# Kernel optimization log

Hardware: AMD Instinct MI355X
Metric: run time of the kernel (lower is better)

The kernel has to match this reference:

```python
import jax, jax.numpy as jnp
import numpy as np

EPS = 1e-6
LN_EPS = 1e-6


def _bd(x, W):
    # Block-diagonal dense: x (B, F) viewed as (B, H, D); W (H, D, D)
    B = x.shape[0]
    H, D, _ = W.shape
    return jnp.einsum('bhd,hde->bhe', x.reshape(B, H, D), W).reshape(B, H * D)


def setup_inputs() -> dict:
    key = jax.random.key(0)
    B, F, H, D, K = 4096, 1024, 4, 256, 4
    ks = jax.random.split(key, 24)
    inp = {}
    inp['inputs'] = jax.random.normal(ks[0], (B, F), jnp.float32)
    inp['c'] = jax.random.normal(ks[1], (B, F), jnp.float32)
    inp['n'] = jax.random.uniform(ks[2], (B, F), jnp.float32)  # nonzero -> general stabilizer branch
    inp['m'] = jax.random.normal(ks[3], (B, F), jnp.float32)
    inp['h'] = jax.random.normal(ks[4], (B, F), jnp.float32)
    inp['conv_state'] = jax.random.normal(ks[5], (B, K, F), jnp.float32)
    inp['conv_kernel'] = jax.random.normal(ks[6], (K, F), jnp.float32) * 0.1
    inp['conv_bias'] = jax.random.normal(ks[7], (F,), jnp.float32) * 0.1
    for idx, name in enumerate(['Wi', 'Wf', 'Wz', 'Wo', 'Ri', 'Rf', 'Rz', 'Ro']):
        inp[name] = jax.random.normal(ks[8 + idx], (H, D, D), jnp.float32) * 0.02
    for idx, name in enumerate(['bi', 'bf', 'bz', 'bo']):
        inp[name] = jax.random.normal(ks[16 + idx], (F,), jnp.float32) * 0.1
    inp['ln_scale'] = jnp.ones((H, D), jnp.float32)
    return inp


def reference(inputs, c, n, m, h, conv_state, conv_kernel, conv_bias,
              Wi, Wf, Wz, Wo, Ri, Rf, Rz, Ro, bi, bf, bz, bo, ln_scale):
    B = inputs.shape[0]
    H, D = ln_scale.shape

    # Causal depthwise conv, single step: shift state, append new input
    new_conv_state = jnp.concatenate([conv_state[:, 1:, :], inputs[:, None, :]], axis=1)  # (B,K,F)
    conv_x = jnp.einsum('bkf,kf->bf', new_conv_state, conv_kernel) + conv_bias
    conv_act = jax.nn.silu(conv_x)

    # Gate pre-activations: input (block-diag) + recurrent (block-diag) + bias
    i = _bd(conv_act, Wi) + _bd(h, Ri) + bi
    f = _bd(conv_act, Wf) + _bd(h, Rf) + bf
    z = _bd(inputs, Wz) + _bd(h, Rz) + bz
    o = _bd(inputs, Wo) + _bd(h, Ro) + bo

    o_gate = jax.nn.sigmoid(o)
    log_f = -jax.nn.softplus(-f)  # forget_activation == 'sigmoid'

    # Stabilizer
    m_new = jnp.where(jnp.all(n == 0.0), i, jnp.maximum(log_f + m, i))
    i_p = jnp.minimum(jnp.exp(i - m_new), 1.0)
    f_p = jnp.minimum(jnp.exp(log_f + m - m_new), 1.0)

    c_new = f_p * c + i_p * jnp.tanh(z)
    n_new = f_p * n + i_p
    h_new = o_gate * (c_new / jnp.maximum(n_new, EPS))

    # Multi-head LayerNorm over head_dim (scale only, no bias)
    y = h_new.reshape(B, H, D)
    mu = jnp.mean(y, axis=-1, keepdims=True)
    var = jnp.var(y, axis=-1, keepdims=True)
    out = ((y - mu) * jax.lax.rsqrt(var + LN_EPS) * ln_scale).reshape(B, H * D)

    return (out, c_new, n_new, m_new, h_new, new_conv_state)
```

## Files before the change

### kernel.cpp

```cpp
#include <hip/hip_runtime.h>

#define B_N 4096
#define F_N 1024
#define H_N 4
#define D_N 256
#define BF_ELEMS (B_N * F_N)

typedef unsigned short u16;
typedef __bf16 bf16x8 __attribute__((ext_vector_type(8)));
typedef float f32x4 __attribute__((ext_vector_type(4)));
typedef u16 u16x4 __attribute__((ext_vector_type(4)));

__device__ __forceinline__ u16 f2bf(float v) {
    union { float f; unsigned u; } x; x.f = v;
    unsigned r = x.u + 0x7fffu + ((x.u >> 16) & 1u);
    return (u16)(r >> 16);
}

__device__ __forceinline__ float bf2f(u16 v) {
    union { unsigned u; float f; } x; x.u = ((unsigned)v) << 16;
    return x.f;
}

__global__ __launch_bounds__(256) void kprep(
    const float* __restrict__ inputs, const float* __restrict__ cs,
    const float* __restrict__ ck, const float* __restrict__ cb,
    const float* __restrict__ h, const float* __restrict__ n,
    const float* W0, const float* W1, const float* W2, const float* W3,
    const float* W4, const float* W5, const float* W6, const float* W7,
    float* __restrict__ ncs_out, u16* __restrict__ convact,
    u16* __restrict__ hbf, u16* __restrict__ inbf,
    u16* __restrict__ wt, int* __restrict__ flag) {
    __shared__ float tile[32][33];
    int bid = blockIdx.x;
    int t = threadIdx.x;
    if (bid < 4096) {
        int idx = bid * 256 + t;
        int flat = idx << 2;
        int b = flat >> 10;
        int f = flat & 1023;
        const f32x4 x  = *(const f32x4*)(inputs + flat);
        const f32x4 c1 = *(const f32x4*)(cs + b * 4096 + 1024 + f);
        const f32x4 c2 = *(const f32x4*)(cs + b * 4096 + 2048 + f);
        const f32x4 c3 = *(const f32x4*)(cs + b * 4096 + 3072 + f);
        const f32x4 k0 = *(const f32x4*)(ck + f);
        const f32x4 k1 = *(const f32x4*)(ck + 1024 + f);
        const f32x4 k2 = *(const f32x4*)(ck + 2048 + f);
        const f32x4 k3 = *(const f32x4*)(ck + 3072 + f);
        const f32x4 bias = *(const f32x4*)(cb + f);
        const f32x4 h4 = *(const f32x4*)(h + flat);
        const f32x4 nv = *(const f32x4*)(n + flat);

        bool any = (nv[0] != 0.f) || (nv[1] != 0.f) || (nv[2] != 0.f) || (nv[3] != 0.f);
        unsigned long long msk = __ballot(any);
        if (msk && (t & 63) == 0) *flag = 1;

        u16x4 ca, hb, ib;
        #pragma unroll
        for (int q = 0; q < 4; ++q) {
            float v = c1[q] * k0[q] + c2[q] * k1[q] + c3[q] * k2[q] + x[q] * k3[q] + bias[q];
            float a = v / (1.f + expf(-v));
            ca[q] = f2bf(a);
            hb[q] = f2bf(h4[q]);
            ib[q] = f2bf(x[q]);
        }
        *(u16x4*)(convact + flat) = ca;
        *(u16x4*)(hbf + flat) = hb;
        *(u16x4*)(inbf + flat) = ib;

        float* ob = ncs_out + b * 4096 + f;
        *(f32x4*)(ob)        = c1;
        *(f32x4*)(ob + 1024) = c2;
        *(f32x4*)(ob + 2048) = c3;
        *(f32x4*)(ob + 3072) = x;
    } else {
        int wb = bid - 4096;
        int gx = wb & 63;
        int hd = (wb >> 6) & 3;
        int mat = wb >> 8;
        const float* tab[8] = {W0, W1, W2, W3, W4, W5, W6, W7};
        const float* src = tab[mat] + hd * 65536;
        u16* dst = wt + (mat * 4 + hd) * 65536;
        int tx = t & 31, ty = t >> 5;
        int bx = (gx & 7) * 32;
        int by = (gx >> 3) * 32;
        #pragma unroll
        for (int r = 0; r < 4; ++r)
            tile[ty + r * 8][tx] = src[(by + ty + r * 8) * 256 + bx + tx];
        __syncthreads();
        #pragma unroll
        for (int r = 0; r < 4; ++r)
            dst[(bx + ty + r * 8) * 256 + by + tx] = f2bf(tile[tx][ty + r * 8]);
    }
}

__global__ __launch_bounds__(512, 4) void kgemm(
    const u16* __restrict__ convact, const u16* __restrict__ inbf,
    const u16* __restrict__ hbf, const u16* __restrict__ wt,
    const float* __restrict__ bgi, const float* __restrict__ bgf,
    const float* __restrict__ bgz, const float* __restrict__ bgo,
    u16* __restrict__ gates16) {
    __shared__ u16 ldsA[128 * 64];
    __shared__ u16 ldsB[256 * 64];

    int t = threadIdx.x;
    int mtile = blockIdx.x;
    int pairidx = blockIdx.y;
    int gsel = pairidx >> 2;
    int hd = pairidx & 3;
    int row0 = mtile * 128;

    const u16* a0 = (gsel >= 2 ? inbf : convact) + row0 * 1024 + hd * 256;
    const u16* a1 = hbf + row0 * 1024 + hd * 256;
    const u16* b0 = wt + (gsel * 4 + hd) * 65536;
    const u16* b1 = wt + ((gsel + 4) * 4 + hd) * 65536;
    const float* bias = (gsel == 0 ? bgi : gsel == 1 ? bgf : gsel == 2 ? bgz : bgo) + hd * 256;

    f32x4 acc[4][4];
    #pragma unroll
    for (int i = 0; i < 4; ++i)
        #pragma unroll
        for (int j = 0; j < 4; ++j)
            acc[i][j] = (f32x4){0.f, 0.f, 0.f, 0.f};

    int lane = t & 63;
    int lr = lane & 15, lk = lane >> 4;
    int w = t >> 6;
    int wm = w >> 2, wn = w & 3;
    int wbase = t & ~63;

    int arow = t >> 3, aseg = t & 7;

    for (int ks = 0; ks < 8; ++ks) {
        int kb = ks * 64;
        const u16* ap = (kb < 256) ? (a0 + kb) : (a1 + (kb - 256));
        const u16* bp = (kb < 256) ? (b0 + kb) : (b1 + (kb - 256));
        __syncthreads();
        #pragma unroll
        for (int s = 0; s < 2; ++s) {
            int row = arow + s * 64;
            __builtin_amdgcn_global_load_lds(
                (const __attribute__((address_space(1))) void*)(ap + row * 1024 + aseg * 8),
                (__attribute__((address_space(3))) void*)(&ldsA[(wbase + s * 512) * 8]),
                16, 0, 0);
        }
        #pragma unroll
        for (int s = 0; s < 4; ++s) {
            int row = arow + s * 64;
            __builtin_amdgcn_global_load_lds(
                (const __attribute__((address_space(1))) void*)(bp + row * 256 + aseg * 8),
                (__attribute__((address_space(3))) void*)(&ldsB[(wbase + s * 512) * 8]),
                16, 0, 0);
        }
        __syncthreads();

        #pragma unroll
        for (int kk = 0; kk < 2; ++kk) {
            bf16x8 a[4], bfr[4];
            #pragma unroll
            for (int mi = 0; mi < 4; ++mi)
                a[mi] = *(const bf16x8*)&ldsA[(wm * 64 + mi * 16 + lr) * 64 + kk * 32 + lk * 8];
            #pragma unroll
            for (int ni = 0; ni < 4; ++ni)
                bfr[ni] = *(const bf16x8*)&ldsB[(wn * 64 + ni * 16 + lr) * 64 + kk * 32 + lk * 8];
            #pragma unroll
            for (int mi = 0; mi < 4; ++mi)
                #pragma unroll
                for (int ni = 0; ni < 4; ++ni)
                    acc[mi][ni] = __builtin_amdgcn_mfma_f32_16x16x32_bf16(a[mi], bfr[ni], acc[mi][ni], 0, 0, 0);
        }
    }

    float bv[4];
    #pragma unroll
    for (int ni = 0; ni < 4; ++ni)
        bv[ni] = bias[wn * 64 + ni * 16 + lr];

    u16* gout = gates16 + (size_t)gsel * BF_ELEMS;
    #pragma unroll
    for (int mi = 0; mi < 4; ++mi)
        #pragma unroll
        for (int ni = 0; ni < 4; ++ni)
            #pragma unroll
            for (int r = 0; r < 4; ++r) {
                int row = row0 + wm * 64 + mi * 16 + lk * 4 + r;
                int col = hd * 256 + wn * 64 + ni * 16 + lr;
                gout[row * 1024 + col] = f2bf(acc[mi][ni][r] + bv[ni]);
            }
}

__global__ __launch_bounds__(256) void kpoint(
    const u16* __restrict__ gates16,
    const float* __restrict__ c, const float* __restrict__ n, const float* __restrict__ m,
    const float* __restrict__ ln_scale, const int* __restrict__ flagp,
    float* __restrict__ out) {
    int b = blockIdx.x;
    int t = threadIdx.x;
    int l = t & 63;
    int j = (t >> 6) * 256 + l * 4;
    int idx = b * 1024 + j;
    int flag = *flagp;

    u16x4 iv = *(const u16x4*)(gates16 + idx);
    u16x4 fv = *(const u16x4*)(gates16 + (size_t)BF_ELEMS + idx);
    u16x4 zv = *(const u16x4*)(gates16 + 2 * (size_t)BF_ELEMS + idx);
    u16x4 ov = *(const u16x4*)(gates16 + 3 * (size_t)BF_ELEMS + idx);
    f32x4 cv = *(const f32x4*)(c + idx);
    f32x4 nv = *(const f32x4*)(n + idx);
    f32x4 mv = *(const f32x4*)(m + idx);
    f32x4 sc = *(const f32x4*)(ln_scale + j);

    f32x4 cn, nn, mn, hn;
    float s = 0.f, ss = 0.f;
    #pragma unroll
    for (int q = 0; q < 4; ++q) {
        float I = bf2f(iv[q]);
        float Fg = bf2f(fv[q]);
        float Z = bf2f(zv[q]);
        float O = bf2f(ov[q]);
        float og = 1.f / (1.f + expf(-O));
        float lf = (Fg >= 0.f) ? -log1pf(expf(-Fg)) : (Fg - log1pf(expf(Fg)));
        float mnew = flag ? fmaxf(lf + mv[q], I) : I;
        float ip = fminf(expf(I - mnew), 1.f);
        float fp = fminf(expf(lf + mv[q] - mnew), 1.f);
        float cnew = fp * cv[q] + ip * tanhf(Z);
        float nnew = fp * nv[q] + ip;
        float hnew = og * (cnew / fmaxf(nnew, 1e-6f));
        cn[q] = cnew; nn[q] = nnew; mn[q] = mnew; hn[q] = hnew;
        s += hnew; ss += hnew * hnew;
    }
    #pragma unroll
    for (int off = 32; off >= 1; off >>= 1) {
        s  += __shfl_xor(s, off);
        ss += __shfl_xor(ss, off);
    }
    float mu = s * (1.f / 256.f);
    float var = ss * (1.f / 256.f) - mu * mu;
    float rs = rsqrtf(var + 1e-6f);

    f32x4 o4;
    #pragma unroll
    for (int q = 0; q < 4; ++q)
        o4[q] = (hn[q] - mu) * rs * sc[q];

    *(f32x4*)(out + idx) = o4;
    *(f32x4*)(out + (size_t)BF_ELEMS + idx) = cn;
    *(f32x4*)(out + 2 * (size_t)BF_ELEMS + idx) = nn;
    *(f32x4*)(out + 3 * (size_t)BF_ELEMS + idx) = mn;
    *(f32x4*)(out + 4 * (size_t)BF_ELEMS + idx) = hn;
}

extern "C" void kernel_launch(void* const* d_in, const int* in_sizes, int n_in,
                              void* d_out, int out_size, void* d_ws, size_t ws_size,
                              hipStream_t stream) {
    const float* inputs = (const float*)d_in[0];
    const float* c = (const float*)d_in[1];
    const float* n = (const float*)d_in[2];
    const float* m = (const float*)d_in[3];
    const float* h = (const float*)d_in[4];
    const float* conv_state = (const float*)d_in[5];
    const float* conv_kernel = (const float*)d_in[6];
    const float* conv_bias = (const float*)d_in[7];
    const float* W[8];
    for (int i = 0; i < 8; ++i) W[i] = (const float*)d_in[8 + i];
    const float* bgi = (const float*)d_in[16];
    const float* bgf = (const float*)d_in[17];
    const float* bgz = (const float*)d_in[18];
    const float* bgo = (const float*)d_in[19];
    const float* ln_scale = (const float*)d_in[20];
    float* out = (float*)d_out;

    char* ws = (char*)d_ws;
    int* flag = (int*)ws;
    u16* convact = (u16*)(ws + 256);
    u16* hbf = convact + BF_ELEMS;
    u16* inbf = hbf + BF_ELEMS;
    u16* wt = inbf + BF_ELEMS;
    u16* gates16 = wt + (size_t)8 * 4 * 65536;

    hipMemsetAsync(flag, 0, 4, stream);
    kprep<<<6144, 256, 0, stream>>>(inputs, conv_state, conv_kernel, conv_bias, h, n,
                                    W[0], W[1], W[2], W[3], W[4], W[5], W[6], W[7],
                                    out + 5 * (size_t)BF_ELEMS, convact, hbf, inbf, wt, flag);
    kgemm<<<dim3(32, 16), 512, 0, stream>>>(convact, inbf, hbf, wt,
                                            bgi, bgf, bgz, bgo, gates16);
    kpoint<<<4096, 256, 0, stream>>>(gates16, c, n, m, ln_scale, flag, out);
}
```

Baseline: 114.4 us.

## Double-buffer GEMM LDS tiles, enlarge M tile to 256, add XOR swizzle

The gate GEMM kernel now prefetches the next K tile into a second LDS buffer while computing on the current one, removing one barrier per iteration. The M tile doubles to 256 rows per block, so each wave handles 8x4 MFMA tiles and half as many blocks launch. An XOR swizzle on the LDS column segments is meant to avoid bank conflicts on fragment reads. In exchange it uses 128KB of LDS, more accumulator registers and lower occupancy (launch bounds cut to 2), and only 256 blocks run across the CUs.

```diff
diff --git a/kernel.cpp b/kernel.cpp
--- a/kernel.cpp
+++ b/kernel.cpp
@@ -94,21 +94,21 @@
     }
 }
 
-__global__ __launch_bounds__(512, 4) void kgemm(
+__global__ __launch_bounds__(512, 2) void kgemm(
     const u16* __restrict__ convact, const u16* __restrict__ inbf,
     const u16* __restrict__ hbf, const u16* __restrict__ wt,
     const float* __restrict__ bgi, const float* __restrict__ bgf,
     const float* __restrict__ bgz, const float* __restrict__ bgo,
     u16* __restrict__ gates16) {
-    __shared__ u16 ldsA[128 * 64];
-    __shared__ u16 ldsB[256 * 64];
+    __shared__ u16 ldsA[2][256 * 64];
+    __shared__ u16 ldsB[2][256 * 64];
 
     int t = threadIdx.x;
     int mtile = blockIdx.x;
     int pairidx = blockIdx.y;
     int gsel = pairidx >> 2;
     int hd = pairidx & 3;
-    int row0 = mtile * 128;
+    int row0 = mtile * 256;
 
     const u16* a0 = (gsel >= 2 ? inbf : convact) + row0 * 1024 + hd * 256;
     const u16* a1 = hbf + row0 * 1024 + hd * 256;
@@ -116,9 +116,9 @@
     const u16* b1 = wt + ((gsel + 4) * 4 + hd) * 65536;
     const float* bias = (gsel == 0 ? bgi : gsel == 1 ? bgf : gsel == 2 ? bgz : bgo) + hd * 256;
 
-    f32x4 acc[4][4];
-    #pragma unroll
-    for (int i = 0; i < 4; ++i)
+    f32x4 acc[8][4];
+    #pragma unroll
+    for (int i = 0; i < 8; ++i)
         #pragma unroll
         for (int j = 0; j < 4; ++j)
             acc[i][j] = (f32x4){0.f, 0.f, 0.f, 0.f};
@@ -128,47 +128,58 @@
     int w = t >> 6;
     int wm = w >> 2, wn = w & 3;
     int wbase = t & ~63;
-
-    int arow = t >> 3, aseg = t & 7;
-
-    for (int ks = 0; ks < 8; ++ks) {
-        int kb = ks * 64;
-        const u16* ap = (kb < 256) ? (a0 + kb) : (a1 + (kb - 256));
-        const u16* bp = (kb < 256) ? (b0 + kb) : (b1 + (kb - 256));
-        __syncthreads();
-        #pragma unroll
-        for (int s = 0; s < 2; ++s) {
-            int row = arow + s * 64;
-            __builtin_amdgcn_global_load_lds(
-                (const __attribute__((address_space(1))) void*)(ap + row * 1024 + aseg * 8),
-                (__attribute__((address_space(3))) void*)(&ldsA[(wbase + s * 512) * 8]),
-                16, 0, 0);
-        }
-        #pragma unroll
-        for (int s = 0; s < 4; ++s) {
-            int row = arow + s * 64;
-            __builtin_amdgcn_global_load_lds(
-                (const __attribute__((address_space(1))) void*)(bp + row * 256 + aseg * 8),
-                (__attribute__((address_space(3))) void*)(&ldsB[(wbase + s * 512) * 8]),
-                16, 0, 0);
+    int srow = t >> 3;
+    int gsw = (t & 7) ^ ((t >> 3) & 7);
+
+    #define STAGE_TILE(buf, kt) do {                                              \
+        int kb = (kt) * 64;                                                       \
+        const u16* ap = (kb < 256) ? (a0 + kb) : (a1 + (kb - 256));               \
+        const u16* bp = (kb < 256) ? (b0 + kb) : (b1 + (kb - 256));               \
+        _Pragma("unroll")                                                         \
+        for (int s = 0; s < 4; ++s) {                                             \
+            int row = srow + s * 64;                                              \
+            __builtin_amdgcn_global_load_lds(                                     \
+                (const __attribute__((address_space(1))) void*)(ap + row * 1024 + gsw * 8), \
+                (__attribute__((address_space(3))) void*)(&ldsA[buf][(s * 512 + wbase) * 8]), \
+                16, 0, 0);                                                        \
+        }                                                                         \
+        _Pragma("unroll")                                                         \
+        for (int s = 0; s < 4; ++s) {                                             \
+            int row = srow + s * 64;                                              \
+            __builtin_amdgcn_global_load_lds(                                     \
+                (const __attribute__((address_space(1))) void*)(bp + row * 256 + gsw * 8), \
+                (__attribute__((address_space(3))) void*)(&ldsB[buf][(s * 512 + wbase) * 8]), \
+                16, 0, 0);                                                        \
+        }                                                                         \
+    } while (0)
+
+    STAGE_TILE(0, 0);
+    __syncthreads();
+
+    for (int kt = 0; kt < 8; ++kt) {
+        int buf = kt & 1;
+        if (kt < 7) STAGE_TILE(buf ^ 1, kt + 1);
+
+        #pragma unroll
+        for (int kk = 0; kk < 2; ++kk) {
+            bf16x8 a[8], bb[4];
+            #pragma unroll
+            for (int mi = 0; mi < 8; ++mi) {
+                int row = wm * 128 + mi * 16 + lr;
+                a[mi] = *(const bf16x8*)&ldsA[buf][row * 64 + (((kk * 4 + lk) ^ (lr & 7)) * 8)];
+            }
+            #pragma unroll
+            for (int ni = 0; ni < 4; ++ni) {
+                int row = wn * 64 + ni * 16 + lr;
+                bb[ni] = *(const bf16x8*)&ldsB[buf][row * 64 + (((kk * 4 + lk) ^ (lr & 7)) * 8)];
+            }
+            #pragma unroll
+            for (int mi = 0; mi < 8; ++mi)
+                #pragma unroll
+                for (int ni = 0; ni < 4; ++ni)
+                    acc[mi][ni] = __builtin_amdgcn_mfma_f32_16x16x32_bf16(a[mi], bb[ni], acc[mi][ni], 0, 0, 0);
         }
         __syncthreads();
-
-        #pragma unroll
-        for (int kk = 0; kk < 2; ++kk) {
-            bf16x8 a[4], bfr[4];
-            #pragma unroll
-            for (int mi = 0; mi < 4; ++mi)
-                a[mi] = *(const bf16x8*)&ldsA[(wm * 64 + mi * 16 + lr) * 64 + kk * 32 + lk * 8];
-            #pragma unroll
-            for (int ni = 0; ni < 4; ++ni)
-                bfr[ni] = *(const bf16x8*)&ldsB[(wn * 64 + ni * 16 + lr) * 64 + kk * 32 + lk * 8];
-            #pragma unroll
-            for (int mi = 0; mi < 4; ++mi)
-                #pragma unroll
-                for (int ni = 0; ni < 4; ++ni)
-                    acc[mi][ni] = __builtin_amdgcn_mfma_f32_16x16x32_bf16(a[mi], bfr[ni], acc[mi][ni], 0, 0, 0);
-        }
     }
 
     float bv[4];
@@ -178,15 +189,16 @@
 
     u16* gout = gates16 + (size_t)gsel * BF_ELEMS;
     #pragma unroll
-    for (int mi = 0; mi < 4; ++mi)
+    for (int mi = 0; mi < 8; ++mi)
         #pragma unroll
         for (int ni = 0; ni < 4; ++ni)
             #pragma unroll
             for (int r = 0; r < 4; ++r) {
-                int row = row0 + wm * 64 + mi * 16 + lk * 4 + r;
+                int row = row0 + wm * 128 + mi * 16 + lk * 4 + r;
                 int col = hd * 256 + wn * 64 + ni * 16 + lr;
                 gout[row * 1024 + col] = f2bf(acc[mi][ni][r] + bv[ni]);
             }
+    #undef STAGE_TILE
 }
 
 __global__ __launch_bounds__(256) void kpoint(
@@ -282,7 +294,7 @@
     kprep<<<6144, 256, 0, stream>>>(inputs, conv_state, conv_kernel, conv_bias, h, n,
                                     W[0], W[1], W[2], W[3], W[4], W[5], W[6], W[7],
                                     out + 5 * (size_t)BF_ELEMS, convact, hbf, inbf, wt, flag);
-    kgemm<<<dim3(32, 16), 512, 0, stream>>>(convact, inbf, hbf, wt,
+    kgemm<<<dim3(16, 16), 512, 0, stream>>>(convact, inbf, hbf, wt,
                                             bgi, bgf, bgz, bgo, gates16);
     kpoint<<<4096, 256, 0, stream>>>(gates16, c, n, m, ln_scale, flag, out);
 }
```

New measurement: 112.4 us. No clear change (-1.7%).

## Fuse gate GEMMs with pointwise cell update and LayerNorm per head tile

Applied to the files above, without the earlier changes.

Merges the gate GEMM and pointwise kernels into one kernel. Each block computes all four gates for a 32-row by one-head tile, stages the bf16 gate values in LDS, then runs the stabilized cell update and per-head LayerNorm directly. This removes the global round trip of the bf16 gates buffer and one kernel launch. Weights are rearranged into k-chunked panels and read straight from global/L2 into registers rather than through LDS. Activations are loaded once into swizzled LDS. The cost is that every block re-reads the full weight panels from cache, and the grid is smaller with 1024-thread blocks.

```diff
diff --git a/kernel.cpp b/kernel.cpp
--- a/kernel.cpp
+++ b/kernel.cpp
@@ -10,6 +10,7 @@
 typedef __bf16 bf16x8 __attribute__((ext_vector_type(8)));
 typedef float f32x4 __attribute__((ext_vector_type(4)));
 typedef u16 u16x4 __attribute__((ext_vector_type(4)));
+typedef u16 u16x8 __attribute__((ext_vector_type(8)));
 
 __device__ __forceinline__ u16 f2bf(float v) {
     union { float f; unsigned u; } x; x.f = v;
@@ -90,164 +91,180 @@
         __syncthreads();
         #pragma unroll
         for (int r = 0; r < 4; ++r)
-            dst[(bx + ty + r * 8) * 256 + by + tx] = f2bf(tile[tx][ty + r * 8]);
-    }
-}
-
-__global__ __launch_bounds__(512, 4) void kgemm(
+            dst[(by >> 5) * 8192 + (bx + ty + r * 8) * 32 + tx] = f2bf(tile[tx][ty + r * 8]);
+    }
+}
+
+__global__ __launch_bounds__(1024, 4) void kfused(
     const u16* __restrict__ convact, const u16* __restrict__ inbf,
-    const u16* __restrict__ hbf, const u16* __restrict__ wt,
+    const u16* __restrict__ hbf, const u16* __restrict__ wt2,
     const float* __restrict__ bgi, const float* __restrict__ bgf,
     const float* __restrict__ bgz, const float* __restrict__ bgo,
-    u16* __restrict__ gates16) {
-    __shared__ u16 ldsA[128 * 64];
-    __shared__ u16 ldsB[256 * 64];
+    const float* __restrict__ c, const float* __restrict__ n,
+    const float* __restrict__ m, const float* __restrict__ ln_scale,
+    const int* __restrict__ flagp, float* __restrict__ out) {
+    __shared__ __align__(16) u16 smem[32768];
 
     int t = threadIdx.x;
     int mtile = blockIdx.x;
-    int pairidx = blockIdx.y;
-    int gsel = pairidx >> 2;
-    int hd = pairidx & 3;
-    int row0 = mtile * 128;
-
-    const u16* a0 = (gsel >= 2 ? inbf : convact) + row0 * 1024 + hd * 256;
-    const u16* a1 = hbf + row0 * 1024 + hd * 256;
-    const u16* b0 = wt + (gsel * 4 + hd) * 65536;
-    const u16* b1 = wt + ((gsel + 4) * 4 + hd) * 65536;
-    const float* bias = (gsel == 0 ? bgi : gsel == 1 ? bgf : gsel == 2 ? bgz : bgo) + hd * 256;
-
-    f32x4 acc[4][4];
+    int hd = blockIdx.y;
+    int row0 = mtile * 32;
+
+    {
+        int r = t >> 5, gd = t & 31;
+        int gl = gd ^ (r & 7);
+        size_t soff = (size_t)(row0 + r) * 1024 + hd * 256 + gl * 8;
+        __builtin_amdgcn_global_load_lds(
+            (const __attribute__((address_space(1))) void*)(convact + soff),
+            (__attribute__((address_space(3))) void*)(&smem[t * 8]), 16, 0, 0);
+        __builtin_amdgcn_global_load_lds(
+            (const __attribute__((address_space(1))) void*)(inbf + soff),
+            (__attribute__((address_space(3))) void*)(&smem[8192 + t * 8]), 16, 0, 0);
+        __builtin_amdgcn_global_load_lds(
+            (const __attribute__((address_space(1))) void*)(hbf + soff),
+            (__attribute__((address_space(3))) void*)(&smem[16384 + t * 8]), 16, 0, 0);
+    }
+    __syncthreads();
+
+    int lane = t & 63, lr = lane & 15, lk = lane >> 4;
+    int w = t >> 6;
+    int g = w >> 2;
+    int q = w & 3;
+
+    f32x4 acc[2][4];
     #pragma unroll
-    for (int i = 0; i < 4; ++i)
+    for (int i = 0; i < 2; ++i)
         #pragma unroll
         for (int j = 0; j < 4; ++j)
             acc[i][j] = (f32x4){0.f, 0.f, 0.f, 0.f};
 
-    int lane = t & 63;
-    int lr = lane & 15, lk = lane >> 4;
-    int w = t >> 6;
-    int wm = w >> 2, wn = w & 3;
-    int wbase = t & ~63;
-
-    int arow = t >> 3, aseg = t & 7;
-
+    const u16* bW = wt2 + (size_t)(g * 4 + hd) * 65536;
+    const u16* bR = wt2 + (size_t)((g + 4) * 4 + hd) * 65536;
+    int bcol = (q * 64 + lr) * 32 + lk * 8;
+    int aselW = (g < 2) ? 0 : 8192;
+    int grs = (lr & 7);
+
+    #pragma unroll 4
     for (int ks = 0; ks < 8; ++ks) {
-        int kb = ks * 64;
-        const u16* ap = (kb < 256) ? (a0 + kb) : (a1 + (kb - 256));
-        const u16* bp = (kb < 256) ? (b0 + kb) : (b1 + (kb - 256));
-        __syncthreads();
-        #pragma unroll
-        for (int s = 0; s < 2; ++s) {
-            int row = arow + s * 64;
-            __builtin_amdgcn_global_load_lds(
-                (const __attribute__((address_space(1))) void*)(ap + row * 1024 + aseg * 8),
-                (__attribute__((address_space(3))) void*)(&ldsA[(wbase + s * 512) * 8]),
-                16, 0, 0);
-        }
-        #pragma unroll
-        for (int s = 0; s < 4; ++s) {
-            int row = arow + s * 64;
-            __builtin_amdgcn_global_load_lds(
-                (const __attribute__((address_space(1))) void*)(bp + row * 256 + aseg * 8),
-                (__attribute__((address_space(3))) void*)(&ldsB[(wbase + s * 512) * 8]),
-                16, 0, 0);
-        }
-        __syncthreads();
-
-        #pragma unroll
-        for (int kk = 0; kk < 2; ++kk) {
-            bf16x8 a[4], bfr[4];
+        bf16x8 b0 = *(const bf16x8*)(bW + ks * 8192 + bcol);
+        bf16x8 b1 = *(const bf16x8*)(bW + ks * 8192 + bcol + 512);
+        bf16x8 b2 = *(const bf16x8*)(bW + ks * 8192 + bcol + 1024);
+        bf16x8 b3 = *(const bf16x8*)(bW + ks * 8192 + bcol + 1536);
+        int gr = (ks * 4 + lk) ^ grs;
+        bf16x8 a0 = *(const bf16x8*)&smem[aselW + lr * 256 + gr * 8];
+        bf16x8 a1 = *(const bf16x8*)&smem[aselW + (16 + lr) * 256 + gr * 8];
+        acc[0][0] = __builtin_amdgcn_mfma_f32_16x16x32_bf16(a0, b0, acc[0][0], 0, 0, 0);
+        acc[0][1] = __builtin_amdgcn_mfma_f32_16x16x32_bf16(a0, b1, acc[0][1], 0, 0, 0);
+        acc[0][2] = __builtin_amdgcn_mfma_f32_16x16x32_bf16(a0, b2, acc[0][2], 0, 0, 0);
+        acc[0][3] = __builtin_amdgcn_mfma_f32_16x16x32_bf16(a0, b3, acc[0][3], 0, 0, 0);
+        acc[1][0] = __builtin_amdgcn_mfma_f32_16x16x32_bf16(a1, b0, acc[1][0], 0, 0, 0);
+        acc[1][1] = __builtin_amdgcn_mfma_f32_16x16x32_bf16(a1, b1, acc[1][1], 0, 0, 0);
+        acc[1][2] = __builtin_amdgcn_mfma_f32_16x16x32_bf16(a1, b2, acc[1][2], 0, 0, 0);
+        acc[1][3] = __builtin_amdgcn_mfma_f32_16x16x32_bf16(a1, b3, acc[1][3], 0, 0, 0);
+    }
+    #pragma unroll 4
+    for (int ks = 0; ks < 8; ++ks) {
+        bf16x8 b0 = *(const bf16x8*)(bR + ks * 8192 + bcol);
+        bf16x8 b1 = *(const bf16x8*)(bR + ks * 8192 + bcol + 512);
+        bf16x8 b2 = *(const bf16x8*)(bR + ks * 8192 + bcol + 1024);
+        bf16x8 b3 = *(const bf16x8*)(bR + ks * 8192 + bcol + 1536);
+        int gr = (ks * 4 + lk) ^ grs;
+        bf16x8 a0 = *(const bf16x8*)&smem[16384 + lr * 256 + gr * 8];
+        bf16x8 a1 = *(const bf16x8*)&smem[16384 + (16 + lr) * 256 + gr * 8];
+        acc[0][0] = __builtin_amdgcn_mfma_f32_16x16x32_bf16(a0, b0, acc[0][0], 0, 0, 0);
+        acc[0][1] = __builtin_amdgcn_mfma_f32_16x16x32_bf16(a0, b1, acc[0][1], 0, 0, 0);
+        acc[0][2] = __builtin_amdgcn_mfma_f32_16x16x32_bf16(a0, b2, acc[0][2], 0, 0, 0);
+        acc[0][3] = __builtin_amdgcn_mfma_f32_16x16x32_bf16(a0, b3, acc[0][3], 0, 0, 0);
+        acc[1][0] = __builtin_amdgcn_mfma_f32_16x16x32_bf16(a1, b0, acc[1][0], 0, 0, 0);
+        acc[1][1] = __builtin_amdgcn_mfma_f32_16x16x32_bf16(a1, b1, acc[1][1], 0, 0, 0);
+        acc[1][2] = __builtin_amdgcn_mfma_f32_16x16x32_bf16(a1, b2, acc[1][2], 0, 0, 0);
+        acc[1][3] = __builtin_amdgcn_mfma_f32_16x16x32_bf16(a1, b3, acc[1][3], 0, 0, 0);
+    }
+
+    __syncthreads();
+    {
+        const float* bt = (g == 0 ? bgi : g == 1 ? bgf : g == 2 ? bgz : bgo)
+                          + hd * 256 + q * 64;
+        #pragma unroll
+        for (int nt = 0; nt < 4; ++nt) {
+            float bv = bt[nt * 16 + lr];
+            int col = g * 256 + q * 64 + nt * 16 + lr;
             #pragma unroll
-            for (int mi = 0; mi < 4; ++mi)
-                a[mi] = *(const bf16x8*)&ldsA[(wm * 64 + mi * 16 + lr) * 64 + kk * 32 + lk * 8];
-            #pragma unroll
-            for (int ni = 0; ni < 4; ++ni)
-                bfr[ni] = *(const bf16x8*)&ldsB[(wn * 64 + ni * 16 + lr) * 64 + kk * 32 + lk * 8];
-            #pragma unroll
-            for (int mi = 0; mi < 4; ++mi)
+            for (int mt = 0; mt < 2; ++mt)
                 #pragma unroll
-                for (int ni = 0; ni < 4; ++ni)
-                    acc[mi][ni] = __builtin_amdgcn_mfma_f32_16x16x32_bf16(a[mi], bfr[ni], acc[mi][ni], 0, 0, 0);
-        }
-    }
-
-    float bv[4];
-    #pragma unroll
-    for (int ni = 0; ni < 4; ++ni)
-        bv[ni] = bias[wn * 64 + ni * 16 + lr];
-
-    u16* gout = gates16 + (size_t)gsel * BF_ELEMS;
-    #pragma unroll
-    for (int mi = 0; mi < 4; ++mi)
-        #pragma unroll
-        for (int ni = 0; ni < 4; ++ni)
-            #pragma unroll
-            for (int r = 0; r < 4; ++r) {
-                int row = row0 + wm * 64 + mi * 16 + lk * 4 + r;
-                int col = hd * 256 + wn * 64 + ni * 16 + lr;
-                gout[row * 1024 + col] = f2bf(acc[mi][ni][r] + bv[ni]);
-            }
-}
-
-__global__ __launch_bounds__(256) void kpoint(
-    const u16* __restrict__ gates16,
-    const float* __restrict__ c, const float* __restrict__ n, const float* __restrict__ m,
-    const float* __restrict__ ln_scale, const int* __restrict__ flagp,
-    float* __restrict__ out) {
-    int b = blockIdx.x;
-    int t = threadIdx.x;
-    int l = t & 63;
-    int j = (t >> 6) * 256 + l * 4;
-    int idx = b * 1024 + j;
-    int flag = *flagp;
-
-    u16x4 iv = *(const u16x4*)(gates16 + idx);
-    u16x4 fv = *(const u16x4*)(gates16 + (size_t)BF_ELEMS + idx);
-    u16x4 zv = *(const u16x4*)(gates16 + 2 * (size_t)BF_ELEMS + idx);
-    u16x4 ov = *(const u16x4*)(gates16 + 3 * (size_t)BF_ELEMS + idx);
-    f32x4 cv = *(const f32x4*)(c + idx);
-    f32x4 nv = *(const f32x4*)(n + idx);
-    f32x4 mv = *(const f32x4*)(m + idx);
-    f32x4 sc = *(const f32x4*)(ln_scale + j);
-
-    f32x4 cn, nn, mn, hn;
-    float s = 0.f, ss = 0.f;
-    #pragma unroll
-    for (int q = 0; q < 4; ++q) {
-        float I = bf2f(iv[q]);
-        float Fg = bf2f(fv[q]);
-        float Z = bf2f(zv[q]);
-        float O = bf2f(ov[q]);
-        float og = 1.f / (1.f + expf(-O));
-        float lf = (Fg >= 0.f) ? -log1pf(expf(-Fg)) : (Fg - log1pf(expf(Fg)));
-        float mnew = flag ? fmaxf(lf + mv[q], I) : I;
-        float ip = fminf(expf(I - mnew), 1.f);
-        float fp = fminf(expf(lf + mv[q] - mnew), 1.f);
-        float cnew = fp * cv[q] + ip * tanhf(Z);
-        float nnew = fp * nv[q] + ip;
-        float hnew = og * (cnew / fmaxf(nnew, 1e-6f));
-        cn[q] = cnew; nn[q] = nnew; mn[q] = mnew; hn[q] = hnew;
-        s += hnew; ss += hnew * hnew;
-    }
-    #pragma unroll
-    for (int off = 32; off >= 1; off >>= 1) {
-        s  += __shfl_xor(s, off);
-        ss += __shfl_xor(ss, off);
-    }
-    float mu = s * (1.f / 256.f);
-    float var = ss * (1.f / 256.f) - mu * mu;
-    float rs = rsqrtf(var + 1e-6f);
-
-    f32x4 o4;
-    #pragma unroll
-    for (int q = 0; q < 4; ++q)
-        o4[q] = (hn[q] - mu) * rs * sc[q];
-
-    *(f32x4*)(out + idx) = o4;
-    *(f32x4*)(out + (size_t)BF_ELEMS + idx) = cn;
-    *(f32x4*)(out + 2 * (size_t)BF_ELEMS + idx) = nn;
-    *(f32x4*)(out + 3 * (size_t)BF_ELEMS + idx) = mn;
-    *(f32x4*)(out + 4 * (size_t)BF_ELEMS + idx) = hn;
+                for (int r = 0; r < 4; ++r)
+                    smem[(mt * 16 + lk * 4 + r) * 1024 + col] = f2bf(acc[mt][nt][r] + bv);
+        }
+    }
+    __syncthreads();
+
+    {
+        int prow = t >> 5;
+        int e0 = (t & 31) * 8;
+        u16x8 iv = *(const u16x8*)&smem[prow * 1024 + e0];
+        u16x8 fv = *(const u16x8*)&smem[prow * 1024 + 256 + e0];
+        u16x8 zv = *(const u16x8*)&smem[prow * 1024 + 512 + e0];
+        u16x8 ov = *(const u16x8*)&smem[prow * 1024 + 768 + e0];
+        size_t idx = (size_t)(row0 + prow) * 1024 + hd * 256 + e0;
+        f32x4 cv0 = *(const f32x4*)(c + idx), cv1 = *(const f32x4*)(c + idx + 4);
+        f32x4 nv0 = *(const f32x4*)(n + idx), nv1 = *(const f32x4*)(n + idx + 4);
+        f32x4 mv0 = *(const f32x4*)(m + idx), mv1 = *(const f32x4*)(m + idx + 4);
+        f32x4 sc0 = *(const f32x4*)(ln_scale + hd * 256 + e0);
+        f32x4 sc1 = *(const f32x4*)(ln_scale + hd * 256 + e0 + 4);
+        int flag = *flagp;
+
+        float cn[8], nn[8], mn[8], hn[8];
+        float s = 0.f, ss = 0.f;
+        #pragma unroll
+        for (int e = 0; e < 8; ++e) {
+            float I = bf2f(iv[e]);
+            float Fg = bf2f(fv[e]);
+            float Z = bf2f(zv[e]);
+            float O = bf2f(ov[e]);
+            float cvq = (e < 4) ? cv0[e] : cv1[e - 4];
+            float nvq = (e < 4) ? nv0[e] : nv1[e - 4];
+            float mvq = (e < 4) ? mv0[e] : mv1[e - 4];
+            float og = 1.f / (1.f + expf(-O));
+            float lf = (Fg >= 0.f) ? -log1pf(expf(-Fg)) : (Fg - log1pf(expf(Fg)));
+            float mnew = flag ? fmaxf(lf + mvq, I) : I;
+            float ip = fminf(expf(I - mnew), 1.f);
+            float fp = fminf(expf(lf + mvq - mnew), 1.f);
+            float cnew = fp * cvq + ip * tanhf(Z);
+            float nnew = fp * nvq + ip;
+            float hnew = og * (cnew / fmaxf(nnew, 1e-6f));
+            cn[e] = cnew; nn[e] = nnew; mn[e] = mnew; hn[e] = hnew;
+            s += hnew; ss += hnew * hnew;
+        }
+        #pragma unroll
+        for (int off = 16; off >= 1; off >>= 1) {
+            s  += __shfl_xor(s, off);
+            ss += __shfl_xor(ss, off);
+        }
+        float mu = s * (1.f / 256.f);
+        float var = ss * (1.f / 256.f) - mu * mu;
+        float rs = rsqrtf(var + 1e-6f);
+
+        f32x4 o0, o1, c0, c1, n0, n1, m0, m1, h0, h1;
+        #pragma unroll
+        for (int e = 0; e < 4; ++e) {
+            o0[e] = (hn[e] - mu) * rs * sc0[e];
+            o1[e] = (hn[e + 4] - mu) * rs * sc1[e];
+            c0[e] = cn[e]; c1[e] = cn[e + 4];
+            n0[e] = nn[e]; n1[e] = nn[e + 4];
+            m0[e] = mn[e]; m1[e] = mn[e + 4];
+            h0[e] = hn[e]; h1[e] = hn[e + 4];
+        }
+        *(f32x4*)(out + idx) = o0;
+        *(f32x4*)(out + idx + 4) = o1;
+        *(f32x4*)(out + (size_t)BF_ELEMS + idx) = c0;
+        *(f32x4*)(out + (size_t)BF_ELEMS + idx + 4) = c1;
+        *(f32x4*)(out + 2 * (size_t)BF_ELEMS + idx) = n0;
+        *(f32x4*)(out + 2 * (size_t)BF_ELEMS + idx + 4) = n1;
+        *(f32x4*)(out + 3 * (size_t)BF_ELEMS + idx) = m0;
+        *(f32x4*)(out + 3 * (size_t)BF_ELEMS + idx + 4) = m1;
+        *(f32x4*)(out + 4 * (size_t)BF_ELEMS + idx) = h0;
+        *(f32x4*)(out + 4 * (size_t)BF_ELEMS + idx + 4) = h1;
+    }
 }
 
 extern "C" void kernel_launch(void* const* d_in, const int* in_sizes, int n_in,
@@ -275,14 +292,13 @@
     u16* convact = (u16*)(ws + 256);
     u16* hbf = convact + BF_ELEMS;
     u16* inbf = hbf + BF_ELEMS;
-    u16* wt = inbf + BF_ELEMS;
-    u16* gates16 = wt + (size_t)8 * 4 * 65536;
+    u16* wt2 = inbf + BF_ELEMS;
 
     hipMemsetAsync(flag, 0, 4, stream);
     kprep<<<6144, 256, 0, stream>>>(inputs, conv_state, conv_kernel, conv_bias, h, n,
                                     W[0], W[1], W[2], W[3], W[4], W[5], W[6], W[7],
-                                    out + 5 * (size_t)BF_ELEMS, convact, hbf, inbf, wt, flag);
-    kgemm<<<dim3(32, 16), 512, 0, stream>>>(convact, inbf, hbf, wt,
-                                            bgi, bgf, bgz, bgo, gates16);
-    kpoint<<<4096, 256, 0, stream>>>(gates16, c, n, m, ln_scale, flag, out);
-}
+                                    out + 5 * (size_t)BF_ELEMS, convact, hbf, inbf, wt2, flag);
+    kfused<<<dim3(128, 4), 1024, 0, stream>>>(convact, inbf, hbf, wt2,
+                                              bgi, bgf, bgz, bgo,
+                                              c, n, m, ln_scale, flag, out);
+}
```

After: 128.8 us. 12.6% more time.
